# Kernel tuning notes

Measured on AMD Instinct MI355X. Metric: run time of the kernel, lower is better.

## Reference

```python
import jax, jax.numpy as jnp
import numpy as np

N = 100000   # nodes
E = 1600000  # edges
G = 64       # graphs in batch
D = 128      # node_dim
H = 128      # hid_dim
OUT = 10     # out_dim (classes)
L = 3        # max_layer GIN layers per branch
BN_EPS = 1e-5


def setup_inputs() -> dict:
    key = jax.random.key(0)
    ks = jax.random.split(key, 24)
    p = lambda k, shape: (jax.random.normal(k, shape, jnp.float32) * 0.05)
    inp = {
        "x": jax.random.normal(ks[0], (N, D), jnp.float32),
        "edge_index": jax.random.randint(ks[1], (2, E), 0, N, jnp.int32),
        "batch": jnp.sort(jax.random.randint(ks[2], (N,), 0, G, jnp.int32)),
        # branch A: conv1 + convs  (stacked per-layer params; node_dim == hid_dim)
        "W1a": p(ks[3], (L, D, H)), "b1a": p(ks[4], (L, H)),
        "W2a": p(ks[5], (L, H, H)), "b2a": p(ks[6], (L, H)),
        "ga": jnp.ones((L, H), jnp.float32), "bta": jnp.zeros((L, H), jnp.float32),
        # branch B: conv2 + convs2
        "W1b": p(ks[7], (L, D, H)), "b1b": p(ks[8], (L, H)),
        "W2b": p(ks[9], (L, H, H)), "b2b": p(ks[10], (L, H)),
        "gb": jnp.ones((L, H), jnp.float32), "btb": jnp.zeros((L, H), jnp.float32),
        # heads
        "lin1_w": p(ks[11], (2 * H, H)), "lin1_b": p(ks[12], (H,)),
        "lin2_w": p(ks[13], (H, OUT)), "lin2_b": p(ks[14], (OUT,)),
        # bilinear discriminator (nn.Bilinear(H, H, 1))
        "disc_w": p(ks[15], (H, H)), "disc_b": jnp.zeros((), jnp.float32),
    }
    return inp


def _gin(h, src, dst, W1, b1, W2, b2, g, bt):
    # GINConv (eps=0): MLP(x + sum_{j->i} x_j); MLP = Lin-ReLU-Lin-ReLU-BN
    agg = jax.ops.segment_sum(h[src], dst, num_segments=N)  # scatter-add over edges
    h = h + agg
    h = jax.nn.relu(h @ W1 + b1)
    h = jax.nn.relu(h @ W2 + b2)
    mu = h.mean(0)
    var = jnp.mean((h - mu) ** 2, axis=0)
    return (h - mu) * jax.lax.rsqrt(var + BN_EPS) * g + bt


def reference(x, edge_index, batch, W1a, b1a, W2a, b2a, ga, bta,
              W1b, b1b, W2b, b2b, gb, btb, lin1_w, lin1_b, lin2_w, lin2_b,
              disc_w, disc_b):
    src, dst = edge_index[0], edge_index[1]
    counts = jnp.clip(jax.ops.segment_sum(jnp.ones((N,), x.dtype), batch, num_segments=G), 1.0)

    # branch A: conv1 + convs -> per-graph mean pool
    h = x
    for i in range(L):
        h = _gin(h, src, dst, W1a[i], b1a[i], W2a[i], b2a[i], ga[i], bta[i])
    mean_a = jax.ops.segment_sum(h, batch, num_segments=G) / counts[:, None]  # [G,H]

    # branch B (subgraph branch, run on the same graph): conv2 + convs2 -> pool
    hb = x
    for i in range(L):
        hb = _gin(hb, src, dst, W1b[i], b1b[i], W2b[i], b2b[i], gb[i], btb[i])
    pool_x = jax.ops.segment_sum(hb, batch, num_segments=G) / counts[:, None]  # [G,H]

    # MI discriminator: shuffle index as in Net.MI
    idx = jnp.arange(G - 1, -1, -1)
    idx = idx.at[G // 2].set(idx[G // 2 + 1])
    shuffled = pool_x[idx]
    bil = lambda a, c: jnp.einsum('gd,de,ge->g', a, disc_w, c) + disc_b
    logits = jnp.concatenate([bil(pool_x, pool_x), bil(pool_x, shuffled)])  # [2G]

    # classification head: cat(mean_pool, pool_x) -> lin1 -> relu -> lin2 -> log_softmax
    z = jnp.concatenate([mean_a, pool_x], axis=-1)
    z = jax.nn.relu(z @ lin1_w + lin1_b)
    z = z @ lin2_w + lin2_b
    predicts = jax.nn.log_softmax(z, axis=-1)  # [G,OUT]

    return jnp.concatenate([predicts.ravel(), logits.ravel()])  # [G*OUT + 2G]
```

## Files before the change

kernel.cpp:

```cpp
#include <hip/hip_runtime.h>
#include <hip/hip_bf16.h>

#define NN 100000
#define EE 1600000
#define GG 64
#define HH 128
#define LL 3
#define BN_EPS 1e-5f
#define NBUCK 196
#define BCAP 12288
#define PART_CHUNK 8192
#define NREP 16

typedef __attribute__((ext_vector_type(8))) short bf16x8;
typedef __attribute__((ext_vector_type(4))) float f32x4;
typedef unsigned int uint32;

__device__ __forceinline__ unsigned short f2bf(float f) {
    uint32 x = __float_as_uint(f);
    uint32 r = (x + 0x7fffu + ((x >> 16) & 1u)) >> 16;
    return (unsigned short)r;
}
__device__ __forceinline__ float bf2f(unsigned short u) { return __uint_as_float(((uint32)u) << 16); }
__device__ __forceinline__ void accq(float4& a, uint32 u, float sc) {
    a.x += sc * (float)(u & 0xffu);
    a.y += sc * (float)((u >> 8) & 0xffu);
    a.z += sc * (float)((u >> 16) & 0xffu);
    a.w += sc * (float)(u >> 24);
}
__device__ __forceinline__ void accqs(float4& a, uint32 u, float sc) {
    a.x += sc * (float)((int)(u << 24) >> 24);
    a.y += sc * (float)((int)(u << 16) >> 24);
    a.z += sc * (float)((int)(u << 8) >> 24);
    a.w += sc * (float)((int)u >> 24);
}

__global__ __launch_bounds__(256) void partition_kernel(
    const int* __restrict__ src, const int* __restrict__ dst,
    int* __restrict__ bcnt, uint32* __restrict__ part) {
    __shared__ int cnt[NBUCK];
    __shared__ int loff[NBUCK + 1];
    __shared__ int gpos[NBUCK];
    __shared__ int lcur[NBUCK];
    __shared__ uint32 buf[PART_CHUNK];
    int tid = threadIdx.x;
    int base = blockIdx.x * PART_CHUNK;
    int n = min(PART_CHUNK, EE - base);
    for (int i = tid; i < NBUCK; i += 256) { cnt[i] = 0; lcur[i] = 0; }
    __syncthreads();
    for (int i = tid; i < n; i += 256) atomicAdd(&cnt[dst[base + i] >> 9], 1);
    __syncthreads();
    if (tid == 0) {
        int acc = 0;
        for (int b = 0; b < NBUCK; ++b) { loff[b] = acc; acc += cnt[b]; }
        loff[NBUCK] = acc;
    }
    __syncthreads();
    if (tid < NBUCK && cnt[tid] > 0) gpos[tid] = atomicAdd(&bcnt[tid], cnt[tid]);
    __syncthreads();
    for (int i = tid; i < n; i += 256) {
        int d = dst[base + i];
        int s = src[base + i];
        int b = d >> 9;
        int slot = atomicAdd(&lcur[b], 1);
        buf[loff[b] + slot] = (uint32)s | ((uint32)(d & 511) << 17);
    }
    __syncthreads();
    for (int i = tid; i < n; i += 256) {
        int lo = 0, hi = NBUCK;
        while (hi - lo > 1) { int mid = (lo + hi) >> 1; if (loff[mid] <= i) lo = mid; else hi = mid; }
        part[(size_t)lo * BCAP + gpos[lo] + (i - loff[lo])] = buf[i];
    }
}

__global__ __launch_bounds__(256) void build_col_kernel(
    const uint32* __restrict__ part, const int* __restrict__ bcnt,
    int* __restrict__ col, int2* __restrict__ rowpair) {
    __shared__ int ldeg[512];
    __shared__ int loffn[512];
    __shared__ int lcur[512];
    __shared__ int pscan[256];
    __shared__ int cl[BCAP];
    int b = blockIdx.x;
    int tid = threadIdx.x;
    int node0 = b << 9;
    int nn = min(node0 + 512, NN) - node0;
    int cnt = bcnt[b];
    int base = b * BCAP;
    const uint32* pp = part + (size_t)base;
    for (int i = tid; i < 512; i += 256) { ldeg[i] = 0; lcur[i] = 0; }
    __syncthreads();
    for (int i = tid; i < cnt; i += 256) atomicAdd(&ldeg[pp[i] >> 17], 1);
    __syncthreads();
    int t2 = tid * 2;
    int a0 = ldeg[t2], a1 = ldeg[t2 + 1];
    int ps = a0 + a1;
    pscan[tid] = ps;
    __syncthreads();
    for (int off = 1; off < 256; off <<= 1) {
        int v = (tid >= off) ? pscan[tid - off] : 0;
        __syncthreads();
        pscan[tid] += v;
        __syncthreads();
    }
    int eo = pscan[tid] - ps;
    loffn[t2] = eo;
    loffn[t2 + 1] = eo + a0;
    if (t2 < nn)     rowpair[node0 + t2]     = make_int2(base + eo, base + eo + a0);
    if (t2 + 1 < nn) rowpair[node0 + t2 + 1] = make_int2(base + eo + a0, base + eo + a0 + a1);
    __syncthreads();
    for (int i = tid; i < cnt; i += 256) {
        uint32 v = pp[i];
        int dl = (int)(v >> 17);
        int pos = atomicAdd(&lcur[dl], 1);
        cl[loffn[dl] + pos] = (int)(v & 0x1FFFFu);
    }
    __syncthreads();
    for (int i = tid; i < cnt; i += 256) col[base + i] = cl[i];
}

__global__ void counts_kernel(const int* __restrict__ batch, float* __restrict__ cnt, int n) {
    __shared__ int h[GG];
    int tid = threadIdx.x;
    if (tid < GG) h[tid] = 0;
    __syncthreads();
    int i = blockIdx.x * 256 + tid;
    if (i < n) atomicAdd(&h[batch[i]], 1);
    __syncthreads();
    if (tid < GG && h[tid]) atomicAdd(&cnt[tid], (float)h[tid]);
}

__global__ void x_to_i8_kernel(const float* __restrict__ x, unsigned short* __restrict__ x8,
                               float* __restrict__ sc0) {
    int row = (blockIdx.x * 256 + threadIdx.x) >> 6;
    int lane = threadIdx.x & 63;
    if (row >= NN) return;
    float2 v = ((const float2*)x)[(size_t)row * 64 + lane];
    float m = fmaxf(fabsf(v.x), fabsf(v.y));
#pragma unroll
    for (int off = 1; off < 64; off <<= 1) m = fmaxf(m, __shfl_xor(m, off));
    float scale = m * (1.f / 127.f);
    float inv = (m > 0.f) ? 127.f / m : 0.f;
    int b0 = __float2int_rn(v.x * inv);
    int b1 = __float2int_rn(v.y * inv);
    unsigned short pk = (unsigned short)((b0 & 0xff) | ((b1 & 0xff) << 8));
    x8[(size_t)row * 64 + lane] = pk;
    if (lane == 0) sc0[row] = scale;
}

#define MAT_STRIDE 16384

__global__ void convert_w_kernel(const float* __restrict__ W1a, const float* __restrict__ W2a,
                                 const float* __restrict__ W1b, const float* __restrict__ W2b,
                                 unsigned short* __restrict__ out) {
    int t = blockIdx.x * 256 + threadIdx.x;
    if (t >= 24576) return;
    int lane = t & 63;
    int r = t >> 6;
    int ks = r & 3; r >>= 2;
    int nt = r & 7; r >>= 3;
    int mat = r & 1; r >>= 1;
    int l = r % 3, br = r / 3;
    const float* W = br ? (mat ? W2b : W1b) : (mat ? W2a : W1a);
    const float* Wl = W + (size_t)l * 128 * 128;
    int n0 = nt * 16 + (lane & 15);
    int k0 = ks * 32 + (lane >> 4) * 8;
    unsigned short tmp[8];
#pragma unroll
    for (int j = 0; j < 8; ++j) tmp[j] = f2bf(Wl[(size_t)(k0 + j) * 128 + n0]);
    size_t seq = (size_t)(br * 3 + l) * 2 + mat;
    size_t off = (((seq * 8 + nt) * 4 + ks) * 64 + (size_t)lane) * 8;
    *(uint4*)(out + off) = *(const uint4*)tmp;
}

__global__ void bn_coefs_kernel(const float* __restrict__ statsRep,
                                const float* __restrict__ ga, const float* __restrict__ bta,
                                const float* __restrict__ gb, const float* __restrict__ btb,
                                int l, float* __restrict__ coef) {
    int t = threadIdx.x;
    int br = t >> 7, cc = t & 127;
    const float* base = statsRep + (size_t)((l * 2 + br) * NREP) * 256;
    float s = 0.f, sq = 0.f;
#pragma unroll
    for (int rep = 0; rep < NREP; ++rep) {
        s += base[rep * 256 + cc];
        sq += base[rep * 256 + 128 + cc];
    }
    float mu = s * (1.f / NN);
    float var = sq * (1.f / NN) - mu * mu;
    float gm = (br ? gb : ga)[l * 128 + cc];
    float A = gm * rsqrtf(var + BN_EPS);
    float B = (br ? btb : bta)[l * 128 + cc] - mu * A;
    coef[br * 256 + cc] = A;
    coef[br * 256 + 128 + cc] = B;
}

__global__ void gather0_kernel(const uint32* __restrict__ x8, const float* __restrict__ sc0,
                               const int2* __restrict__ rowpair, const int* __restrict__ col,
                               uint2* __restrict__ out) {
    int gw = (blockIdx.x * blockDim.x + threadIdx.x) >> 6;
    int lane = threadIdx.x & 63;
    if (gw >= NN) return;
    int slot = lane >> 5;
    int c = lane & 31;
    float4 accA = {0.f, 0.f, 0.f, 0.f};
    float4 accB = {0.f, 0.f, 0.f, 0.f};
    if (slot == 0) accqs(accA, x8[(size_t)gw * 32 + c], sc0[gw]);
    int2 be = rowpair[gw];
    int beg = be.x, end = be.y;
    for (int base = beg; base < end; base += 64) {
        int nb = min(64, end - base);
        int colv = col[base + min(lane, nb - 1)];
        int k = 0;
        for (; k + 4 <= nb; k += 4) {
            int j0 = __shfl(colv, k + slot);
            int j1 = __shfl(colv, k + 2 + slot);
            float s0 = sc0[j0], s1 = sc0[j1];
            uint32 u0 = x8[(size_t)j0 * 32 + c];
            uint32 u1 = x8[(size_t)j1 * 32 + c];
            accqs(accA, u0, s0);
            accqs(accB, u1, s1);
        }
        for (; k + 2 <= nb; k += 2) {
            int j = __shfl(colv, k + slot);
            accqs(accA, x8[(size_t)j * 32 + c], sc0[j]);
        }
        if (k < nb) {
            int j = __shfl(colv, k);
            if (slot == 0) accqs(accA, x8[(size_t)j * 32 + c], sc0[j]);
        }
    }
    accA.x += accB.x; accA.y += accB.y; accA.z += accB.z; accA.w += accB.w;
    accA.x += __shfl_xor(accA.x, 32);
    accA.y += __shfl_xor(accA.y, 32);
    accA.z += __shfl_xor(accA.z, 32);
    accA.w += __shfl_xor(accA.w, 32);
    if (slot == 0) {
        uint2 o;
        o.x = (uint32)f2bf(accA.x) | ((uint32)f2bf(accA.y) << 16);
        o.y = (uint32)f2bf(accA.z) | ((uint32)f2bf(accA.w) << 16);
        out[(size_t)gw * 32 + c] = o;
    }
}

__global__ void gather_dual_kernel(const uint32* __restrict__ y8, const float* __restrict__ scales,
                                   const int2* __restrict__ rowpair, const int* __restrict__ col,
                                   const float* __restrict__ coef, uint2* __restrict__ out) {
    int gw = (blockIdx.x * blockDim.x + threadIdx.x) >> 6;
    int lane = threadIdx.x & 63;
    if (gw >= NN) return;
    int br = lane >> 5;
    int c32 = lane & 31;
    float4 A4 = ((const float4*)(coef + br * 256))[c32];
    float4 B4 = ((const float4*)(coef + br * 256 + 128))[c32];
    float4 accA = {0.f, 0.f, 0.f, 0.f};
    float4 accB = {0.f, 0.f, 0.f, 0.f};
    {
        uint32 us = y8[(size_t)gw * 64 + lane];
        accq(accA, us, scales[gw * 2 + br]);
    }
    int2 be = rowpair[gw];
    int beg = be.x, end = be.y;
    float degp1 = (float)(end - beg + 1);
    const float2* sc2 = (const float2*)scales;
    for (int base = beg; base < end; base += 64) {
        int nb = min(64, end - base);
        int colv = col[base + min(lane, nb - 1)];
        int k = 0;
        for (; k + 4 <= nb; k += 4) {
            int j0 = __builtin_amdgcn_readlane(colv, k);
            int j1 = __builtin_amdgcn_readlane(colv, k + 1);
            int j2 = __builtin_amdgcn_readlane(colv, k + 2);
            int j3 = __builtin_amdgcn_readlane(colv, k + 3);
            float2 s0 = sc2[j0];
            float2 s1 = sc2[j1];
            float2 s2 = sc2[j2];
            float2 s3 = sc2[j3];
            uint32 u0 = y8[(size_t)j0 * 64 + lane];
            uint32 u1 = y8[(size_t)j1 * 64 + lane];
            uint32 u2 = y8[(size_t)j2 * 64 + lane];
            uint32 u3 = y8[(size_t)j3 * 64 + lane];
            accq(accA, u0, br ? s0.y : s0.x);
            accq(accB, u1, br ? s1.y : s1.x);
            accq(accA, u2, br ? s2.y : s2.x);
            accq(accB, u3, br ? s3.y : s3.x);
        }
        for (; k < nb; ++k) {
            int j = __builtin_amdgcn_readlane(colv, k);
            float2 s = sc2[j];
            accq(accA, y8[(size_t)j * 64 + lane], br ? s.y : s.x);
        }
    }
    float o0 = A4.x * (accA.x + accB.x) + B4.x * degp1;
    float o1 = A4.y * (accA.y + accB.y) + B4.y * degp1;
    float o2 = A4.z * (accA.z + accB.z) + B4.z * degp1;
    float o3 = A4.w * (accA.w + accB.w) + B4.w * degp1;
    uint2 o;
    o.x = (uint32)f2bf(o0) | ((uint32)f2bf(o1) << 16);
    o.y = (uint32)f2bf(o2) | ((uint32)f2bf(o3) << 16);
    out[(size_t)gw * 64 + lane] = o;
}

#define LDS_W1 16384
#define LDS_HS (8 * 16 * 136)
__global__ __launch_bounds__(512, 4) void mlp_dual_kernel(
    const unsigned short* __restrict__ X, int in_stride, int in_off_mul,
    const unsigned short* __restrict__ wf_all,
    const float* __restrict__ b1a, const float* __restrict__ b1b,
    const float* __restrict__ b2a, const float* __restrict__ b2b,
    int l, int quant,
    unsigned short* __restrict__ Y, unsigned char* __restrict__ Y8,
    float* __restrict__ scales, float* __restrict__ statsRep, int n) {
    extern __shared__ unsigned short lds_all[];
    unsigned short* w1s = lds_all;
    unsigned short (*hs)[16][136] = (unsigned short (*)[16][136])(lds_all + LDS_W1);
    float* ssum = (float*)(lds_all + LDS_W1 + LDS_HS);
    float* ssq = ssum + 128;

    int br = blockIdx.y;
    const unsigned short* Wf = wf_all + (size_t)(br * 3 + l) * 2 * MAT_STRIDE;
    const float* b1 = (br ? b1b : b1a) + l * 128;
    const float* b2 = (br ? b2b : b2a) + l * 128;
    float* statsp = statsRep + (size_t)((l * 2 + br) * NREP + (blockIdx.x & (NREP - 1))) * 256;
    int in_off = in_off_mul * br;

    int tid = threadIdx.x;
    int wv = tid >> 6, lane = tid & 63;
    int quad = lane >> 4, l16 = lane & 15;

    const bf16x8* w2g = (const bf16x8*)(Wf + MAT_STRIDE);

    bf16x8 w2p[2][4];
#pragma unroll
    for (int p = 0; p < 2; ++p)
#pragma unroll
        for (int ks = 0; ks < 4; ++ks) w2p[p][ks] = w2g[(p * 4 + ks) * 64 + lane];

    int row0 = blockIdx.x * 128 + wv * 16;

    bf16x8 aF[4];
    {
        int r = row0 + l16;
        if (r >= n) r = n - 1;
        const unsigned short* xrow = X + (size_t)r * in_stride + in_off;
#pragma unroll
        for (int ks = 0; ks < 4; ++ks) aF[ks] = *(const bf16x8*)(xrow + ks * 32 + quad * 8);
    }

    {
        const uint4* srcp = (const uint4*)Wf;
        uint4* dstp = (uint4*)w1s;
        for (int i = tid; i < 2048; i += 512) dstp[i] = srcp[i];
    }
    if (tid < 128) { ssum[tid] = 0.f; ssq[tid] = 0.f; }
    __syncthreads();

    f32x4 acc1[8];
#pragma unroll
    for (int nt = 0; nt < 8; ++nt) {
        f32x4 c = {0.f, 0.f, 0.f, 0.f};
#pragma unroll
        for (int ks = 0; ks < 4; ++ks) {
            bf16x8 bfrag = *(const bf16x8*)(&w1s[((nt * 4 + ks) * 64 + lane) * 8]);
            c = __builtin_amdgcn_mfma_f32_16x16x32_bf16(aF[ks], bfrag, c, 0, 0, 0);
        }
        acc1[nt] = c;
    }

#pragma unroll
    for (int nt = 0; nt < 8; ++nt) {
        int c0 = nt * 16 + l16;
        float bb = b1[c0];
#pragma unroll
        for (int r = 0; r < 4; ++r) {
            float v = fmaxf(acc1[nt][r] + bb, 0.f);
            hs[wv][quad * 4 + r][c0] = f2bf(v);
        }
    }

    bf16x8 aH[4];
#pragma unroll
    for (int ks = 0; ks < 4; ++ks)
        aH[ks] = *(const bf16x8*)(&hs[wv][l16][ks * 32 + quad * 8]);

    f32x4 acc2_[8];
#pragma unroll
    for (int nt = 0; nt < 8; ++nt) {
        bf16x8 bf0, bf1, bf2, bf3;
        if (nt < 2) { bf0 = w2p[nt][0]; bf1 = w2p[nt][1]; bf2 = w2p[nt][2]; bf3 = w2p[nt][3]; }
        else {
            bf0 = w2g[(nt * 4 + 0) * 64 + lane];
            bf1 = w2g[(nt * 4 + 1) * 64 + lane];
            bf2 = w2g[(nt * 4 + 2) * 64 + lane];
            bf3 = w2g[(nt * 4 + 3) * 64 + lane];
        }
        f32x4 c = {0.f, 0.f, 0.f, 0.f};
        c = __builtin_amdgcn_mfma_f32_16x16x32_bf16(aH[0], bf0, c, 0, 0, 0);
        c = __builtin_amdgcn_mfma_f32_16x16x32_bf16(aH[1], bf1, c, 0, 0, 0);
        c = __builtin_amdgcn_mfma_f32_16x16x32_bf16(aH[2], bf2, c, 0, 0, 0);
        c = __builtin_amdgcn_mfma_f32_16x16x32_bf16(aH[3], bf3, c, 0, 0, 0);
        acc2_[nt] = c;
    }

#pragma unroll
    for (int nt = 0; nt < 8; ++nt) {
        int c0 = nt * 16 + l16;
        float bb = b2[c0];
        float s = 0.f, sq = 0.f;
#pragma unroll
        for (int r = 0; r < 4; ++r) {
            float v = fmaxf(acc2_[nt][r] + bb, 0.f);
            if (row0 + quad * 4 + r >= n) v = 0.f;
            acc2_[nt][r] = v;
            s += v; sq += v * v;
        }
        s += __shfl_xor(s, 16); s += __shfl_xor(s, 32);
        sq += __shfl_xor(sq, 16); sq += __shfl_xor(sq, 32);
        if (quad == 0) { atomicAdd(&ssum[c0], s); atomicAdd(&ssq[c0], sq); }
    }

    unsigned char* hs8 = (unsigned char*)&hs[wv][0][0];
    if (!quant) {
#pragma unroll
        for (int nt = 0; nt < 8; ++nt) {
            int c0 = nt * 16 + l16;
#pragma unroll
            for (int r = 0; r < 4; ++r) hs[wv][quad * 4 + r][c0] = f2bf(acc2_[nt][r]);
        }
        int grow = row0 + l16;
        if (grow < n) {
#pragma unroll
            for (int j = 0; j < 4; ++j) {
                uint4 v = *(const uint4*)(&hs[wv][l16][quad * 32 + j * 8]);
                *(uint4*)(Y + (size_t)grow * 256 + br * 128 + quad * 32 + j * 8) = v;
            }
        }
    } else {
#pragma unroll
        for (int r = 0; r < 4; ++r) {
            float m = acc2_[0][r];
#pragma unroll
            for (int nt = 1; nt < 8; ++nt) m = fmaxf(m, acc2_[nt][r]);
            m = fmaxf(m, __shfl_xor(m, 1));
            m = fmaxf(m, __shfl_xor(m, 2));
            m = fmaxf(m, __shfl_xor(m, 4));
            m = fmaxf(m, __shfl_xor(m, 8));
            float sc = m * (1.f / 255.f);
            float inv = (m > 0.f) ? 255.f / m : 0.f;
            int grow = row0 + quad * 4 + r;
            if (l16 == r && grow < n) scales[grow * 2 + br] = sc;
#pragma unroll
            for (int nt = 0; nt < 8; ++nt) {
                uint32 u = (uint32)__float2int_rn(acc2_[nt][r] * inv);
                hs8[(quad * 4 + r) * 144 + nt * 16 + l16] = (unsigned char)u;
            }
        }
        int grow = row0 + l16;
        if (grow < n) {
            *(uint4*)(Y8 + (size_t)grow * 256 + br * 128 + quad * 32) =
                *(const uint4*)(hs8 + l16 * 144 + quad * 32);
            *(uint4*)(Y8 + (size_t)grow * 256 + br * 128 + quad * 32 + 16) =
                *(const uint4*)(hs8 + l16 * 144 + quad * 32 + 16);
        }
    }
    __syncthreads();
    if (tid < 128) {
        atomicAdd(&statsp[tid], ssum[tid]);
        atomicAdd(&statsp[128 + tid], ssq[tid]);
    }
}

#define POOL_CHUNK 128
__global__ void pool_dual_kernel(const unsigned short* __restrict__ h,
                                 const float* __restrict__ coef2,
                                 const int* __restrict__ batch,
                                 float* __restrict__ poolA, float* __restrict__ poolB, int n) {
    int t = threadIdx.x;
    int br = t >> 7, cc = t & 127;
    float a = coef2[br * 256 + cc];
    float b = coef2[br * 256 + 128 + cc];
    float* pool = br ? poolB : poolA;

    int i0 = blockIdx.x * POOL_CHUNK;
    if (i0 >= n) return;
    int i1 = min(i0 + POOL_CHUNK, n);
    float acc = 0.f;
    int cur = batch[i0];
    for (int i = i0; i < i1; ++i) {
        int g = batch[i];
        if (g != cur) {
            atomicAdd(&pool[cur * 128 + cc], acc);
            acc = 0.f;
            cur = g;
        }
        acc += a * bf2f(h[(size_t)i * 256 + t]) + b;
    }
    atomicAdd(&pool[cur * 128 + cc], acc);
}

__global__ void disc_kernel(const float* __restrict__ poolB, const float* __restrict__ cnt,
                            const float* __restrict__ W, const float* __restrict__ db,
                            float* __restrict__ out) {
    int g = blockIdx.x, e = threadIdx.x;
    __shared__ float rs[128], rh[128];
    float invc = 1.f / fmaxf(cnt[g], 1.f);
    int gs = (g == 32) ? 30 : (63 - g);
    float invcs = 1.f / fmaxf(cnt[gs], 1.f);
    const float* a = poolB + g * 128;
    float t = 0.f;
    for (int d = 0; d < 128; ++d) t += a[d] * W[d * 128 + e];
    t *= invc;
    rs[e] = t * poolB[g * 128 + e] * invc;
    rh[e] = t * poolB[gs * 128 + e] * invcs;
    __syncthreads();
    for (int s = 64; s > 0; s >>= 1) {
        if (e < s) { rs[e] += rs[e + s]; rh[e] += rh[e + s]; }
        __syncthreads();
    }
    if (e == 0) {
        out[GG * 10 + g] = rs[0] + db[0];
        out[GG * 10 + GG + g] = rh[0] + db[0];
    }
}

__global__ void head_kernel(const float* __restrict__ poolA, const float* __restrict__ poolB,
                            const float* __restrict__ cnt,
                            const float* __restrict__ w1, const float* __restrict__ b1,
                            const float* __restrict__ w2, const float* __restrict__ b2,
                            float* __restrict__ out) {
    int g = blockIdx.x, j = threadIdx.x;
    __shared__ float s1[128];
    __shared__ float s2[10];
    __shared__ float lse;
    float invc = 1.f / fmaxf(cnt[g], 1.f);
    const float* ma = poolA + g * 128;
    const float* px = poolB + g * 128;
    float acc = b1[j];
    for (int k = 0; k < 128; ++k) acc += ma[k] * invc * w1[k * 128 + j];
    for (int k = 0; k < 128; ++k) acc += px[k] * invc * w1[(128 + k) * 128 + j];
    s1[j] = fmaxf(acc, 0.f);
    __syncthreads();
    if (j < 10) {
        float a = b2[j];
        for (int k = 0; k < 128; ++k) a += s1[k] * w2[k * 10 + j];
        s2[j] = a;
    }
    __syncthreads();
    if (j == 0) {
        float m = s2[0];
        for (int o = 1; o < 10; ++o) m = fmaxf(m, s2[o]);
        float se = 0.f;
        for (int o = 0; o < 10; ++o) se += expf(s2[o] - m);
        lse = m + logf(se);
    }
    __syncthreads();
    if (j < 10) out[g * 10 + j] = s2[j] - lse;
}

extern "C" void kernel_launch(void* const* d_in, const int* in_sizes, int n_in,
                              void* d_out, int out_size, void* d_ws, size_t ws_size,
                              hipStream_t stream) {
    const float* x     = (const float*)d_in[0];
    const int*   ei    = (const int*)d_in[1];
    const int*   batch = (const int*)d_in[2];
    const float* W1a = (const float*)d_in[3];
    const float* b1a = (const float*)d_in[4];
    const float* W2a = (const float*)d_in[5];
    const float* b2a = (const float*)d_in[6];
    const float* ga  = (const float*)d_in[7];
    const float* bta = (const float*)d_in[8];
    const float* W1b = (const float*)d_in[9];
    const float* b1b = (const float*)d_in[10];
    const float* W2b = (const float*)d_in[11];
    const float* b2b = (const float*)d_in[12];
    const float* gb  = (const float*)d_in[13];
    const float* btb = (const float*)d_in[14];
    const float* lin1_w = (const float*)d_in[15];
    const float* lin1_b = (const float*)d_in[16];
    const float* lin2_w = (const float*)d_in[17];
    const float* lin2_b = (const float*)d_in[18];
    const float* disc_w = (const float*)d_in[19];
    const float* disc_b = (const float*)d_in[20];
    float* out = (float*)d_out;

    const int* src = ei;
    const int* dst = ei + EE;

    size_t o = 0;
    auto take = [&](size_t b) { size_t p = o; o = (o + b + 255) & ~(size_t)255; return p; };
    uint8_t* w = (uint8_t*)d_ws;
    size_t o_x8   = take((size_t)NN * 128);
    size_t o_sc0  = take((size_t)NN * 4);
    size_t o_g0   = take((size_t)NN * 128 * 2);
    size_t o_bufP = take((size_t)NN * 256 * 2);
    size_t o_gbuf = take((size_t)NN * 256 * 2);
    size_t o_y8a  = take((size_t)NN * 256);
    size_t o_y8b  = take((size_t)NN * 256);
    size_t o_scA  = take((size_t)NN * 2 * 4);
    size_t o_scB  = take((size_t)NN * 2 * 4);
    size_t o_wf   = take((size_t)12 * MAT_STRIDE * 2);
    size_t o_col  = take((size_t)NBUCK * BCAP * 4);
    size_t o_part = take((size_t)NBUCK * BCAP * 4);
    size_t o_rowpair = take((size_t)NN * 8);
    size_t o_coef = take((size_t)3 * 2 * 256 * 4);
    size_t zero_begin = o;
    size_t o_bcnt   = take((size_t)NBUCK * 4);
    size_t o_stats  = take((size_t)6 * NREP * 256 * 4);
    size_t o_cnt    = take(GG * 4);
    size_t o_poolA  = take((size_t)GG * 128 * 4);
    size_t o_poolB  = take((size_t)GG * 128 * 4);
    size_t zero_end = o;

    unsigned short* x8 = (unsigned short*)(w + o_x8);
    float* sc0 = (float*)(w + o_sc0);
    uint32* g0 = (uint32*)(w + o_g0);
    unsigned short* bufP = (unsigned short*)(w + o_bufP);
    unsigned short* gbuf = (unsigned short*)(w + o_gbuf);
    unsigned char* y8a = (unsigned char*)(w + o_y8a);
    unsigned char* y8b = (unsigned char*)(w + o_y8b);
    float* scA = (float*)(w + o_scA);
    float* scB = (float*)(w + o_scB);
    unsigned short* wf = (unsigned short*)(w + o_wf);
    int* col = (int*)(w + o_col);
    uint32* part = (uint32*)(w + o_part);
    int2* rowpair = (int2*)(w + o_rowpair);
    float* coef = (float*)(w + o_coef);
    int* bcnt = (int*)(w + o_bcnt);
    float* statsRep = (float*)(w + o_stats);
    float* cnt = (float*)(w + o_cnt);
    float* poolA = (float*)(w + o_poolA);
    float* poolB = (float*)(w + o_poolB);

    hipMemsetAsync(w + zero_begin, 0, zero_end - zero_begin, stream);

    x_to_i8_kernel<<<(NN * 64 + 255) / 256, 256, 0, stream>>>(x, x8, sc0);
    convert_w_kernel<<<(24576 + 255) / 256, 256, 0, stream>>>(W1a, W2a, W1b, W2b, wf);

    partition_kernel<<<(EE + PART_CHUNK - 1) / PART_CHUNK, 256, 0, stream>>>(src, dst, bcnt, part);
    build_col_kernel<<<NBUCK, 256, 0, stream>>>(part, bcnt, col, rowpair);
    counts_kernel<<<(NN + 255) / 256, 256, 0, stream>>>(batch, cnt, NN);

    int gatherBlocks = (NN + 3) / 4;
    dim3 mlpGrid((NN + 127) / 128, 2);
    size_t ldsBytes = (size_t)LDS_W1 * 2 + (size_t)LDS_HS * 2 + 256 * 4;

    gather0_kernel<<<gatherBlocks, 256, 0, stream>>>((const uint32*)x8, sc0, rowpair, col, (uint2*)g0);

    mlp_dual_kernel<<<mlpGrid, 512, ldsBytes, stream>>>(
        (const unsigned short*)g0, 128, 0, wf, b1a, b1b, b2a, b2b, 0, 1,
        nullptr, y8a, scA, statsRep, NN);
    bn_coefs_kernel<<<1, 256, 0, stream>>>(statsRep, ga, bta, gb, btb, 0, coef + 0 * 512);

    gather_dual_kernel<<<gatherBlocks, 256, 0, stream>>>(
        (const uint32*)y8a, scA, rowpair, col, coef + 0 * 512, (uint2*)gbuf);
    mlp_dual_kernel<<<mlpGrid, 512, ldsBytes, stream>>>(
        gbuf, 256, 128, wf, b1a, b1b, b2a, b2b, 1, 1,
        nullptr, y8b, scB, statsRep, NN);
    bn_coefs_kernel<<<1, 256, 0, stream>>>(statsRep, ga, bta, gb, btb, 1, coef + 1 * 512);

    gather_dual_kernel<<<gatherBlocks, 256, 0, stream>>>(
        (const uint32*)y8b, scB, rowpair, col, coef + 1 * 512, (uint2*)gbuf);
    mlp_dual_kernel<<<mlpGrid, 512, ldsBytes, stream>>>(
        gbuf, 256, 128, wf, b1a, b1b, b2a, b2b, 2, 0,
        bufP, nullptr, nullptr, statsRep, NN);
    bn_coefs_kernel<<<1, 256, 0, stream>>>(statsRep, ga, bta, gb, btb, 2, coef + 2 * 512);

    pool_dual_kernel<<<(NN + POOL_CHUNK - 1) / POOL_CHUNK, 256, 0, stream>>>(
        bufP, coef + 2 * 512, batch, poolA, poolB, NN);
    disc_kernel<<<GG, 128, 0, stream>>>(poolB, cnt, disc_w, disc_b, out);
    head_kernel<<<GG, 128, 0, stream>>>(poolA, poolB, cnt, lin1_w, lin1_b, lin2_w, lin2_b, out);
}
```

Before: 658.8 us.

## Rework gather kernels to 2-byte-per-lane loads with scalar edge indices and packed FMA

Both gather kernels now have each lane load 2 int8 features per edge (ushort) instead of 4, using wave-uniform scalar loads of column indices in place of shuffles/readlane. The initial quantization is switched to offset-128 unsigned so gather0 uses unsigned conversion and subtracts a summed-scale correction at the end. gather_dual uses v_pk_fma_f32 inline asm to accumulate both branches at once. This aims to cut instruction count and shuffle overhead per edge, at the cost of narrower per-lane memory transactions and a changed output layout that mlp_dual must match.

```diff
diff --git a/kernel.cpp b/kernel.cpp
--- a/kernel.cpp
+++ b/kernel.cpp
@@ -14,6 +14,7 @@
 
 typedef __attribute__((ext_vector_type(8))) short bf16x8;
 typedef __attribute__((ext_vector_type(4))) float f32x4;
+typedef __attribute__((ext_vector_type(2))) float f32x2;
 typedef unsigned int uint32;
 
 __device__ __forceinline__ unsigned short f2bf(float f) {
@@ -22,18 +23,6 @@
     return (unsigned short)r;
 }
 __device__ __forceinline__ float bf2f(unsigned short u) { return __uint_as_float(((uint32)u) << 16); }
-__device__ __forceinline__ void accq(float4& a, uint32 u, float sc) {
-    a.x += sc * (float)(u & 0xffu);
-    a.y += sc * (float)((u >> 8) & 0xffu);
-    a.z += sc * (float)((u >> 16) & 0xffu);
-    a.w += sc * (float)(u >> 24);
-}
-__device__ __forceinline__ void accqs(float4& a, uint32 u, float sc) {
-    a.x += sc * (float)((int)(u << 24) >> 24);
-    a.y += sc * (float)((int)(u << 16) >> 24);
-    a.z += sc * (float)((int)(u << 8) >> 24);
-    a.w += sc * (float)((int)u >> 24);
-}
 
 __global__ __launch_bounds__(256) void partition_kernel(
     const int* __restrict__ src, const int* __restrict__ dst,
@@ -141,8 +130,8 @@
     for (int off = 1; off < 64; off <<= 1) m = fmaxf(m, __shfl_xor(m, off));
     float scale = m * (1.f / 127.f);
     float inv = (m > 0.f) ? 127.f / m : 0.f;
-    int b0 = __float2int_rn(v.x * inv);
-    int b1 = __float2int_rn(v.y * inv);
+    int b0 = __float2int_rn(v.x * inv) + 128;
+    int b1 = __float2int_rn(v.y * inv) + 128;
     unsigned short pk = (unsigned short)((b0 & 0xff) | ((b1 & 0xff) << 8));
     x8[(size_t)row * 64 + lane] = pk;
     if (lane == 0) sc0[row] = scale;
@@ -195,110 +184,107 @@
     coef[br * 256 + 128 + cc] = B;
 }
 
-__global__ void gather0_kernel(const uint32* __restrict__ x8, const float* __restrict__ sc0,
-                               const int2* __restrict__ rowpair, const int* __restrict__ col,
-                               uint2* __restrict__ out) {
+__global__ __launch_bounds__(256) void gather0_kernel(
+    const unsigned short* __restrict__ x8, const float* __restrict__ sc0,
+    const int2* __restrict__ rowpair, const int* __restrict__ col,
+    uint32* __restrict__ out) {
     int gw = (blockIdx.x * blockDim.x + threadIdx.x) >> 6;
     int lane = threadIdx.x & 63;
     if (gw >= NN) return;
-    int slot = lane >> 5;
-    int c = lane & 31;
-    float4 accA = {0.f, 0.f, 0.f, 0.f};
-    float4 accB = {0.f, 0.f, 0.f, 0.f};
-    if (slot == 0) accqs(accA, x8[(size_t)gw * 32 + c], sc0[gw]);
+    gw = __builtin_amdgcn_readfirstlane(gw);
+
+    float a0, a1, b0 = 0.f, b1 = 0.f, S;
+    {
+        float s = sc0[gw];
+        uint32 u = x8[(uint32)gw * 64 + lane];
+        a0 = s * (float)(u & 0xffu);
+        a1 = s * (float)(u >> 8);
+        S = s;
+    }
     int2 be = rowpair[gw];
-    int beg = be.x, end = be.y;
-    for (int base = beg; base < end; base += 64) {
-        int nb = min(64, end - base);
-        int colv = col[base + min(lane, nb - 1)];
-        int k = 0;
-        for (; k + 4 <= nb; k += 4) {
-            int j0 = __shfl(colv, k + slot);
-            int j1 = __shfl(colv, k + 2 + slot);
-            float s0 = sc0[j0], s1 = sc0[j1];
-            uint32 u0 = x8[(size_t)j0 * 32 + c];
-            uint32 u1 = x8[(size_t)j1 * 32 + c];
-            accqs(accA, u0, s0);
-            accqs(accB, u1, s1);
-        }
-        for (; k + 2 <= nb; k += 2) {
-            int j = __shfl(colv, k + slot);
-            accqs(accA, x8[(size_t)j * 32 + c], sc0[j]);
-        }
-        if (k < nb) {
-            int j = __shfl(colv, k);
-            if (slot == 0) accqs(accA, x8[(size_t)j * 32 + c], sc0[j]);
-        }
-    }
-    accA.x += accB.x; accA.y += accB.y; accA.z += accB.z; accA.w += accB.w;
-    accA.x += __shfl_xor(accA.x, 32);
-    accA.y += __shfl_xor(accA.y, 32);
-    accA.z += __shfl_xor(accA.z, 32);
-    accA.w += __shfl_xor(accA.w, 32);
-    if (slot == 0) {
-        uint2 o;
-        o.x = (uint32)f2bf(accA.x) | ((uint32)f2bf(accA.y) << 16);
-        o.y = (uint32)f2bf(accA.z) | ((uint32)f2bf(accA.w) << 16);
-        out[(size_t)gw * 32 + c] = o;
-    }
-}
-
-__global__ void gather_dual_kernel(const uint32* __restrict__ y8, const float* __restrict__ scales,
-                                   const int2* __restrict__ rowpair, const int* __restrict__ col,
-                                   const float* __restrict__ coef, uint2* __restrict__ out) {
+    int beg = __builtin_amdgcn_readfirstlane(be.x);
+    int end = __builtin_amdgcn_readfirstlane(be.y);
+    int k = beg;
+    for (; k + 4 <= end; k += 4) {
+        int j0 = col[k], j1 = col[k + 1], j2 = col[k + 2], j3 = col[k + 3];
+        float s0 = sc0[j0], s1 = sc0[j1], s2 = sc0[j2], s3 = sc0[j3];
+        uint32 u0 = x8[(uint32)j0 * 64 + lane];
+        uint32 u1 = x8[(uint32)j1 * 64 + lane];
+        uint32 u2 = x8[(uint32)j2 * 64 + lane];
+        uint32 u3 = x8[(uint32)j3 * 64 + lane];
+        a0 = fmaf(s0, (float)(u0 & 0xffu), a0); a1 = fmaf(s0, (float)(u0 >> 8), a1);
+        b0 = fmaf(s1, (float)(u1 & 0xffu), b0); b1 = fmaf(s1, (float)(u1 >> 8), b1);
+        a0 = fmaf(s2, (float)(u2 & 0xffu), a0); a1 = fmaf(s2, (float)(u2 >> 8), a1);
+        b0 = fmaf(s3, (float)(u3 & 0xffu), b0); b1 = fmaf(s3, (float)(u3 >> 8), b1);
+        S += (s0 + s1) + (s2 + s3);
+    }
+    for (; k < end; ++k) {
+        int j = col[k];
+        float s = sc0[j];
+        uint32 u = x8[(uint32)j * 64 + lane];
+        a0 = fmaf(s, (float)(u & 0xffu), a0);
+        a1 = fmaf(s, (float)(u >> 8), a1);
+        S += s;
+    }
+    a0 += b0; a1 += b1;
+    a0 -= 128.f * S;
+    a1 -= 128.f * S;
+    out[(uint32)gw * 64 + lane] = (uint32)f2bf(a0) | ((uint32)f2bf(a1) << 16);
+}
+
+__global__ __launch_bounds__(256) void gather_dual_kernel(
+    const unsigned short* __restrict__ y16, const float* __restrict__ scales,
+    const int2* __restrict__ rowpair, const int* __restrict__ col,
+    const float* __restrict__ coef, uint32* __restrict__ out) {
     int gw = (blockIdx.x * blockDim.x + threadIdx.x) >> 6;
     int lane = threadIdx.x & 63;
     if (gw >= NN) return;
-    int br = lane >> 5;
-    int c32 = lane & 31;
-    float4 A4 = ((const float4*)(coef + br * 256))[c32];
-    float4 B4 = ((const float4*)(coef + br * 256 + 128))[c32];
-    float4 accA = {0.f, 0.f, 0.f, 0.f};
-    float4 accB = {0.f, 0.f, 0.f, 0.f};
-    {
-        uint32 us = y8[(size_t)gw * 64 + lane];
-        accq(accA, us, scales[gw * 2 + br]);
-    }
+    gw = __builtin_amdgcn_readfirstlane(gw);
+    const f32x2* sc2 = (const f32x2*)scales;
+
+    f32x2 p0 = {0.f, 0.f}, p1 = {0.f, 0.f};
+    f32x2 q0 = {0.f, 0.f}, q1 = {0.f, 0.f};
+
+    auto edge = [&](int j, f32x2& e0, f32x2& e1) {
+        f32x2 ss = sc2[j];
+        uint32 ua = y16[(uint32)j * 128 + lane];
+        uint32 ub = y16[(uint32)j * 128 + 64 + lane];
+        f32x2 lo = { (float)(ua & 0xffu), (float)(ub & 0xffu) };
+        f32x2 hi = { (float)(ua >> 8),    (float)(ub >> 8) };
+        asm("v_pk_fma_f32 %0, %1, %2, %0" : "+v"(e0) : "v"(lo), "s"(ss));
+        asm("v_pk_fma_f32 %0, %1, %2, %0" : "+v"(e1) : "v"(hi), "s"(ss));
+    };
+
+    edge(gw, p0, p1);
+
     int2 be = rowpair[gw];
-    int beg = be.x, end = be.y;
-    float degp1 = (float)(end - beg + 1);
-    const float2* sc2 = (const float2*)scales;
-    for (int base = beg; base < end; base += 64) {
-        int nb = min(64, end - base);
-        int colv = col[base + min(lane, nb - 1)];
-        int k = 0;
-        for (; k + 4 <= nb; k += 4) {
-            int j0 = __builtin_amdgcn_readlane(colv, k);
-            int j1 = __builtin_amdgcn_readlane(colv, k + 1);
-            int j2 = __builtin_amdgcn_readlane(colv, k + 2);
-            int j3 = __builtin_amdgcn_readlane(colv, k + 3);
-            float2 s0 = sc2[j0];
-            float2 s1 = sc2[j1];
-            float2 s2 = sc2[j2];
-            float2 s3 = sc2[j3];
-            uint32 u0 = y8[(size_t)j0 * 64 + lane];
-            uint32 u1 = y8[(size_t)j1 * 64 + lane];
-            uint32 u2 = y8[(size_t)j2 * 64 + lane];
-            uint32 u3 = y8[(size_t)j3 * 64 + lane];
-            accq(accA, u0, br ? s0.y : s0.x);
-            accq(accB, u1, br ? s1.y : s1.x);
-            accq(accA, u2, br ? s2.y : s2.x);
-            accq(accB, u3, br ? s3.y : s3.x);
-        }
-        for (; k < nb; ++k) {
-            int j = __builtin_amdgcn_readlane(colv, k);
-            float2 s = sc2[j];
-            accq(accA, y8[(size_t)j * 64 + lane], br ? s.y : s.x);
-        }
-    }
-    float o0 = A4.x * (accA.x + accB.x) + B4.x * degp1;
-    float o1 = A4.y * (accA.y + accB.y) + B4.y * degp1;
-    float o2 = A4.z * (accA.z + accB.z) + B4.z * degp1;
-    float o3 = A4.w * (accA.w + accB.w) + B4.w * degp1;
-    uint2 o;
-    o.x = (uint32)f2bf(o0) | ((uint32)f2bf(o1) << 16);
-    o.y = (uint32)f2bf(o2) | ((uint32)f2bf(o3) << 16);
-    out[(size_t)gw * 64 + lane] = o;
+    int beg = __builtin_amdgcn_readfirstlane(be.x);
+    int end = __builtin_amdgcn_readfirstlane(be.y);
+    int k = beg;
+    for (; k + 4 <= end; k += 4) {
+        int j0 = col[k], j1 = col[k + 1], j2 = col[k + 2], j3 = col[k + 3];
+        edge(j0, p0, p1);
+        edge(j1, q0, q1);
+        edge(j2, p0, p1);
+        edge(j3, q0, q1);
+    }
+    for (; k < end; ++k) edge(col[k], p0, p1);
+
+    p0.x += q0.x; p0.y += q0.y;
+    p1.x += q1.x; p1.y += q1.y;
+
+    float dp1 = (float)(end - beg + 1);
+    const f32x2* cf = (const f32x2*)coef;
+    f32x2 mA = cf[lane];
+    f32x2 bA = cf[64 + lane];
+    f32x2 mB = cf[128 + lane];
+    f32x2 bB = cf[192 + lane];
+    float oA0 = mA.x * p0.x + bA.x * dp1;
+    float oA1 = mA.y * p1.x + bA.y * dp1;
+    float oB0 = mB.x * p0.y + bB.x * dp1;
+    float oB1 = mB.y * p1.y + bB.y * dp1;
+    out[(uint32)gw * 128 + lane]      = (uint32)f2bf(oA0) | ((uint32)f2bf(oA1) << 16);
+    out[(uint32)gw * 128 + 64 + lane] = (uint32)f2bf(oB0) | ((uint32)f2bf(oB1) << 16);
 }
 
 #define LDS_W1 16384
@@ -644,7 +630,7 @@
     dim3 mlpGrid((NN + 127) / 128, 2);
     size_t ldsBytes = (size_t)LDS_W1 * 2 + (size_t)LDS_HS * 2 + 256 * 4;
 
-    gather0_kernel<<<gatherBlocks, 256, 0, stream>>>((const uint32*)x8, sc0, rowpair, col, (uint2*)g0);
+    gather0_kernel<<<gatherBlocks, 256, 0, stream>>>(x8, sc0, rowpair, col, g0);
 
     mlp_dual_kernel<<<mlpGrid, 512, ldsBytes, stream>>>(
         (const unsigned short*)g0, 128, 0, wf, b1a, b1b, b2a, b2b, 0, 1,
@@ -652,14 +638,14 @@
     bn_coefs_kernel<<<1, 256, 0, stream>>>(statsRep, ga, bta, gb, btb, 0, coef + 0 * 512);
 
     gather_dual_kernel<<<gatherBlocks, 256, 0, stream>>>(
-        (const uint32*)y8a, scA, rowpair, col, coef + 0 * 512, (uint2*)gbuf);
+        (const unsigned short*)y8a, scA, rowpair, col, coef + 0 * 512, (uint32*)gbuf);
     mlp_dual_kernel<<<mlpGrid, 512, ldsBytes, stream>>>(
         gbuf, 256, 128, wf, b1a, b1b, b2a, b2b, 1, 1,
         nullptr, y8b, scB, statsRep, NN);
     bn_coefs_kernel<<<1, 256, 0, stream>>>(statsRep, ga, bta, gb, btb, 1, coef + 1 * 512);
 
     gather_dual_kernel<<<gatherBlocks, 256, 0, stream>>>(
-        (const uint32*)y8b, scB, rowpair, col, coef + 1 * 512, (uint2*)gbuf);
+        (const unsigned short*)y8b, scB, rowpair, col, coef + 1 * 512, (uint32*)gbuf);
     mlp_dual_kernel<<<mlpGrid, 512, ldsBytes, stream>>>(
         gbuf, 256, 128, wf, b1a, b1b, b2a, b2b, 2, 0,
         bufP, nullptr, nullptr, statsRep, NN);
```

Result: slower. 708.4 us (+7.5%).

## Fuse BN coefficient computation into MLP via last-block counter; offset-int8 gather

Applied to the files above, without the earlier changes.

Removes the three separate bn_coefs kernel launches by having the last block of each mlp_dual grid (detected with an atomic counter and threadfence) reduce the replicated stats and write the BN scale/shift coefficients. Layer-0 node features are now stored as offset-binary uint8 (value+128), so the gather can use the cheaper unsigned unpack and subtract 128*sum(scales) once at the end. Gather kernels also switch to 32-bit byte-offset addressing and launch bounds to reduce address arithmetic. In exchange, the MLP tail gains extra syncs and fences, and the offset correction adds a small rounding difference.

```diff
diff --git a/kernel.cpp b/kernel.cpp
--- a/kernel.cpp
+++ b/kernel.cpp
@@ -28,11 +28,11 @@
     a.z += sc * (float)((u >> 16) & 0xffu);
     a.w += sc * (float)(u >> 24);
 }
-__device__ __forceinline__ void accqs(float4& a, uint32 u, float sc) {
-    a.x += sc * (float)((int)(u << 24) >> 24);
-    a.y += sc * (float)((int)(u << 16) >> 24);
-    a.z += sc * (float)((int)(u << 8) >> 24);
-    a.w += sc * (float)((int)u >> 24);
+__device__ __forceinline__ uint32 ld32(const unsigned char* p, uint32 off) {
+    return *(const uint32*)(p + off);
+}
+__device__ __forceinline__ float ldf(const float* p, uint32 byteoff) {
+    return *(const float*)((const char*)p + byteoff);
 }
 
 __global__ __launch_bounds__(256) void partition_kernel(
@@ -141,8 +141,8 @@
     for (int off = 1; off < 64; off <<= 1) m = fmaxf(m, __shfl_xor(m, off));
     float scale = m * (1.f / 127.f);
     float inv = (m > 0.f) ? 127.f / m : 0.f;
-    int b0 = __float2int_rn(v.x * inv);
-    int b1 = __float2int_rn(v.y * inv);
+    int b0 = __float2int_rn(v.x * inv) + 128;
+    int b1 = __float2int_rn(v.y * inv) + 128;
     unsigned short pk = (unsigned short)((b0 & 0xff) | ((b1 & 0xff) << 8));
     x8[(size_t)row * 64 + lane] = pk;
     if (lane == 0) sc0[row] = scale;
@@ -173,39 +173,25 @@
     *(uint4*)(out + off) = *(const uint4*)tmp;
 }
 
-__global__ void bn_coefs_kernel(const float* __restrict__ statsRep,
-                                const float* __restrict__ ga, const float* __restrict__ bta,
-                                const float* __restrict__ gb, const float* __restrict__ btb,
-                                int l, float* __restrict__ coef) {
-    int t = threadIdx.x;
-    int br = t >> 7, cc = t & 127;
-    const float* base = statsRep + (size_t)((l * 2 + br) * NREP) * 256;
-    float s = 0.f, sq = 0.f;
-#pragma unroll
-    for (int rep = 0; rep < NREP; ++rep) {
-        s += base[rep * 256 + cc];
-        sq += base[rep * 256 + 128 + cc];
-    }
-    float mu = s * (1.f / NN);
-    float var = sq * (1.f / NN) - mu * mu;
-    float gm = (br ? gb : ga)[l * 128 + cc];
-    float A = gm * rsqrtf(var + BN_EPS);
-    float B = (br ? btb : bta)[l * 128 + cc] - mu * A;
-    coef[br * 256 + cc] = A;
-    coef[br * 256 + 128 + cc] = B;
-}
-
-__global__ void gather0_kernel(const uint32* __restrict__ x8, const float* __restrict__ sc0,
-                               const int2* __restrict__ rowpair, const int* __restrict__ col,
-                               uint2* __restrict__ out) {
+__global__ __launch_bounds__(256) void gather0_kernel(
+    const unsigned char* __restrict__ x8b, const float* __restrict__ sc0,
+    const int2* __restrict__ rowpair, const int* __restrict__ col,
+    uint2* __restrict__ out) {
     int gw = (blockIdx.x * blockDim.x + threadIdx.x) >> 6;
     int lane = threadIdx.x & 63;
     if (gw >= NN) return;
     int slot = lane >> 5;
     int c = lane & 31;
+    uint32 c4 = (uint32)c << 2;
     float4 accA = {0.f, 0.f, 0.f, 0.f};
     float4 accB = {0.f, 0.f, 0.f, 0.f};
-    if (slot == 0) accqs(accA, x8[(size_t)gw * 32 + c], sc0[gw]);
+    float S = 0.f;
+    if (slot == 0) {
+        float s = sc0[gw];
+        uint32 u = ld32(x8b, ((uint32)gw << 7) + c4);
+        accq(accA, u, s);
+        S += s;
+    }
     int2 be = rowpair[gw];
     int beg = be.x, end = be.y;
     for (int base = beg; base < end; base += 64) {
@@ -215,19 +201,26 @@
         for (; k + 4 <= nb; k += 4) {
             int j0 = __shfl(colv, k + slot);
             int j1 = __shfl(colv, k + 2 + slot);
-            float s0 = sc0[j0], s1 = sc0[j1];
-            uint32 u0 = x8[(size_t)j0 * 32 + c];
-            uint32 u1 = x8[(size_t)j1 * 32 + c];
-            accqs(accA, u0, s0);
-            accqs(accB, u1, s1);
+            float s0 = ldf(sc0, (uint32)j0 << 2);
+            float s1 = ldf(sc0, (uint32)j1 << 2);
+            uint32 u0 = ld32(x8b, ((uint32)j0 << 7) + c4);
+            uint32 u1 = ld32(x8b, ((uint32)j1 << 7) + c4);
+            accq(accA, u0, s0); S += s0;
+            accq(accB, u1, s1); S += s1;
         }
         for (; k + 2 <= nb; k += 2) {
             int j = __shfl(colv, k + slot);
-            accqs(accA, x8[(size_t)j * 32 + c], sc0[j]);
+            float s = ldf(sc0, (uint32)j << 2);
+            uint32 u = ld32(x8b, ((uint32)j << 7) + c4);
+            accq(accA, u, s); S += s;
         }
         if (k < nb) {
             int j = __shfl(colv, k);
-            if (slot == 0) accqs(accA, x8[(size_t)j * 32 + c], sc0[j]);
+            if (slot == 0) {
+                float s = ldf(sc0, (uint32)j << 2);
+                uint32 u = ld32(x8b, ((uint32)j << 7) + c4);
+                accq(accA, u, s); S += s;
+            }
         }
     }
     accA.x += accB.x; accA.y += accB.y; accA.z += accB.z; accA.w += accB.w;
@@ -235,34 +228,42 @@
     accA.y += __shfl_xor(accA.y, 32);
     accA.z += __shfl_xor(accA.z, 32);
     accA.w += __shfl_xor(accA.w, 32);
+    S += __shfl_xor(S, 32);
+    float f0 = accA.x - 128.f * S;
+    float f1 = accA.y - 128.f * S;
+    float f2 = accA.z - 128.f * S;
+    float f3 = accA.w - 128.f * S;
     if (slot == 0) {
         uint2 o;
-        o.x = (uint32)f2bf(accA.x) | ((uint32)f2bf(accA.y) << 16);
-        o.y = (uint32)f2bf(accA.z) | ((uint32)f2bf(accA.w) << 16);
-        out[(size_t)gw * 32 + c] = o;
-    }
-}
-
-__global__ void gather_dual_kernel(const uint32* __restrict__ y8, const float* __restrict__ scales,
-                                   const int2* __restrict__ rowpair, const int* __restrict__ col,
-                                   const float* __restrict__ coef, uint2* __restrict__ out) {
+        o.x = (uint32)f2bf(f0) | ((uint32)f2bf(f1) << 16);
+        o.y = (uint32)f2bf(f2) | ((uint32)f2bf(f3) << 16);
+        out[(uint32)gw * 32 + c] = o;
+    }
+}
+
+__global__ __launch_bounds__(256) void gather_dual_kernel(
+    const unsigned char* __restrict__ y8, const float* __restrict__ scales,
+    const int2* __restrict__ rowpair, const int* __restrict__ col,
+    const float* __restrict__ coef, uint2* __restrict__ out) {
     int gw = (blockIdx.x * blockDim.x + threadIdx.x) >> 6;
     int lane = threadIdx.x & 63;
     if (gw >= NN) return;
     int br = lane >> 5;
     int c32 = lane & 31;
+    uint32 ln4 = (uint32)lane << 2;
+    uint32 sb4 = (uint32)br << 2;
     float4 A4 = ((const float4*)(coef + br * 256))[c32];
     float4 B4 = ((const float4*)(coef + br * 256 + 128))[c32];
     float4 accA = {0.f, 0.f, 0.f, 0.f};
     float4 accB = {0.f, 0.f, 0.f, 0.f};
     {
-        uint32 us = y8[(size_t)gw * 64 + lane];
-        accq(accA, us, scales[gw * 2 + br]);
+        float s = ldf(scales, ((uint32)gw << 3) + sb4);
+        uint32 u = ld32(y8, ((uint32)gw << 8) + ln4);
+        accq(accA, u, s);
     }
     int2 be = rowpair[gw];
     int beg = be.x, end = be.y;
     float degp1 = (float)(end - beg + 1);
-    const float2* sc2 = (const float2*)scales;
     for (int base = beg; base < end; base += 64) {
         int nb = min(64, end - base);
         int colv = col[base + min(lane, nb - 1)];
@@ -272,23 +273,24 @@
             int j1 = __builtin_amdgcn_readlane(colv, k + 1);
             int j2 = __builtin_amdgcn_readlane(colv, k + 2);
             int j3 = __builtin_amdgcn_readlane(colv, k + 3);
-            float2 s0 = sc2[j0];
-            float2 s1 = sc2[j1];
-            float2 s2 = sc2[j2];
-            float2 s3 = sc2[j3];
-            uint32 u0 = y8[(size_t)j0 * 64 + lane];
-            uint32 u1 = y8[(size_t)j1 * 64 + lane];
-            uint32 u2 = y8[(size_t)j2 * 64 + lane];
-            uint32 u3 = y8[(size_t)j3 * 64 + lane];
-            accq(accA, u0, br ? s0.y : s0.x);
-            accq(accB, u1, br ? s1.y : s1.x);
-            accq(accA, u2, br ? s2.y : s2.x);
-            accq(accB, u3, br ? s3.y : s3.x);
+            float s0 = ldf(scales, ((uint32)j0 << 3) + sb4);
+            float s1 = ldf(scales, ((uint32)j1 << 3) + sb4);
+            float s2 = ldf(scales, ((uint32)j2 << 3) + sb4);
+            float s3 = ldf(scales, ((uint32)j3 << 3) + sb4);
+            uint32 u0 = ld32(y8, ((uint32)j0 << 8) + ln4);
+            uint32 u1 = ld32(y8, ((uint32)j1 << 8) + ln4);
+            uint32 u2 = ld32(y8, ((uint32)j2 << 8) + ln4);
+            uint32 u3 = ld32(y8, ((uint32)j3 << 8) + ln4);
+            accq(accA, u0, s0);
+            accq(accB, u1, s1);
+            accq(accA, u2, s2);
+            accq(accB, u3, s3);
         }
         for (; k < nb; ++k) {
             int j = __builtin_amdgcn_readlane(colv, k);
-            float2 s = sc2[j];
-            accq(accA, y8[(size_t)j * 64 + lane], br ? s.y : s.x);
+            float s = ldf(scales, ((uint32)j << 3) + sb4);
+            uint32 u = ld32(y8, ((uint32)j << 8) + ln4);
+            accq(accA, u, s);
         }
     }
     float o0 = A4.x * (accA.x + accB.x) + B4.x * degp1;
@@ -308,10 +310,14 @@
     const unsigned short* __restrict__ wf_all,
     const float* __restrict__ b1a, const float* __restrict__ b1b,
     const float* __restrict__ b2a, const float* __restrict__ b2b,
+    const float* __restrict__ ga, const float* __restrict__ bta,
+    const float* __restrict__ gb, const float* __restrict__ btb,
     int l, int quant,
     unsigned short* __restrict__ Y, unsigned char* __restrict__ Y8,
-    float* __restrict__ scales, float* __restrict__ statsRep, int n) {
+    float* __restrict__ scales, float* __restrict__ statsRep,
+    float* __restrict__ coefOut, int* __restrict__ ctr, int n) {
     extern __shared__ unsigned short lds_all[];
+    __shared__ int lastFlag;
     unsigned short* w1s = lds_all;
     unsigned short (*hs)[16][136] = (unsigned short (*)[16][136])(lds_all + LDS_W1);
     float* ssum = (float*)(lds_all + LDS_W1 + LDS_HS);
@@ -467,6 +473,33 @@
     if (tid < 128) {
         atomicAdd(&statsp[tid], ssum[tid]);
         atomicAdd(&statsp[128 + tid], ssq[tid]);
+    }
+    __syncthreads();
+    if (tid == 0) {
+        __threadfence();
+        int done = atomicAdd(&ctr[l * 2 + br], 1);
+        lastFlag = (done == (int)gridDim.x - 1) ? 1 : 0;
+    }
+    __syncthreads();
+    if (lastFlag) {
+        __threadfence();
+        if (tid < 128) {
+            const float* sb = statsRep + (size_t)((l * 2 + br) * NREP) * 256;
+            float s = 0.f, sq = 0.f;
+#pragma unroll
+            for (int rep = 0; rep < NREP; ++rep) {
+                s += sb[rep * 256 + tid];
+                sq += sb[rep * 256 + 128 + tid];
+            }
+            float mu = s * (1.f / NN);
+            float var = sq * (1.f / NN) - mu * mu;
+            float gm = (br ? gb : ga)[l * 128 + tid];
+            float A = gm * rsqrtf(var + BN_EPS);
+            float Bv = (br ? btb : bta)[l * 128 + tid] - mu * A;
+            float* cf = coefOut + l * 512 + br * 256;
+            cf[tid] = A;
+            cf[128 + tid] = Bv;
+        }
     }
 }
 
@@ -609,6 +642,7 @@
     size_t o_cnt    = take(GG * 4);
     size_t o_poolA  = take((size_t)GG * 128 * 4);
     size_t o_poolB  = take((size_t)GG * 128 * 4);
+    size_t o_ctr    = take((size_t)8 * 4);
     size_t zero_end = o;
 
     unsigned short* x8 = (unsigned short*)(w + o_x8);
@@ -630,6 +664,7 @@
     float* cnt = (float*)(w + o_cnt);
     float* poolA = (float*)(w + o_poolA);
     float* poolB = (float*)(w + o_poolB);
+    int* ctr = (int*)(w + o_ctr);
 
     hipMemsetAsync(w + zero_begin, 0, zero_end - zero_begin, stream);
 
@@ -644,26 +679,24 @@
     dim3 mlpGrid((NN + 127) / 128, 2);
     size_t ldsBytes = (size_t)LDS_W1 * 2 + (size_t)LDS_HS * 2 + 256 * 4;
 
-    gather0_kernel<<<gatherBlocks, 256, 0, stream>>>((const uint32*)x8, sc0, rowpair, col, (uint2*)g0);
+    gather0_kernel<<<gatherBlocks, 256, 0, stream>>>(
+        (const unsigned char*)x8, sc0, rowpair, col, (uint2*)g0);
 
     mlp_dual_kernel<<<mlpGrid, 512, ldsBytes, stream>>>(
-        (const unsigned short*)g0, 128, 0, wf, b1a, b1b, b2a, b2b, 0, 1,
-        nullptr, y8a, scA, statsRep, NN);
-    bn_coefs_kernel<<<1, 256, 0, stream>>>(statsRep, ga, bta, gb, btb, 0, coef + 0 * 512);
+        (const unsigned short*)g0, 128, 0, wf, b1a, b1b, b2a, b2b,
+        ga, bta, gb, btb, 0, 1, nullptr, y8a, scA, statsRep, coef, ctr, NN);
 
     gather_dual_kernel<<<gatherBlocks, 256, 0, stream>>>(
-        (const uint32*)y8a, scA, rowpair, col, coef + 0 * 512, (uint2*)gbuf);
+        y8a, scA, rowpair, col, coef + 0 * 512, (uint2*)gbuf);
     mlp_dual_kernel<<<mlpGrid, 512, ldsBytes, stream>>>(
-        gbuf, 256, 128, wf, b1a, b1b, b2a, b2b, 1, 1,
-        nullptr, y8b, scB, statsRep, NN);
-    bn_coefs_kernel<<<1, 256, 0, stream>>>(statsRep, ga, bta, gb, btb, 1, coef + 1 * 512);
+        gbuf, 256, 128, wf, b1a, b1b, b2a, b2b,
+        ga, bta, gb, btb, 1, 1, nullptr, y8b, scB, statsRep, coef, ctr, NN);
 
     gather_dual_kernel<<<gatherBlocks, 256, 0, stream>>>(
-        (const uint32*)y8b, scB, rowpair, col, coef + 1 * 512, (uint2*)gbuf);
+        y8b, scB, rowpair, col, coef + 1 * 512, (uint2*)gbuf);
     mlp_dual_kernel<<<mlpGrid, 512, ldsBytes, stream>>>(
-        gbuf, 256, 128, wf, b1a, b1b, b2a, b2b, 2, 0,
-        bufP, nullptr, nullptr, statsRep, NN);
-    bn_coefs_kernel<<<1, 256, 0, stream>>>(statsRep, ga, bta, gb, btb, 2, coef + 2 * 512);
+        gbuf, 256, 128, wf, b1a, b1b, b2a, b2b,
+        ga, bta, gb, btb, 2, 0, bufP, nullptr, nullptr, statsRep, coef, ctr, NN);
 
     pool_dual_kernel<<<(NN + POOL_CHUNK - 1) / POOL_CHUNK, 256, 0, stream>>>(
         bufP, coef + 2 * 512, batch, poolA, poolB, NN);
```

New measurement: 988.1 us. 50.0% more time.
